# Kernel tuning notes

Hardware: AMD Instinct MI355X
Metric: run time of the kernel (lower is better)

Reference implementation:

```python
import jax, jax.numpy as jnp
import numpy as np

DIST_SCALE = 10000.0   # divisor in kernel()
KERNEL_EPS = 0.0001    # additive epsilon before reciprocal


def setup_inputs() -> dict:
    key = jax.random.key(0)
    k1, k2, k3 = jax.random.split(key, 3)
    batch, keysize, dict_size, categories = 4096, 512, 16384, 128
    x = jax.random.normal(k1, (batch, keysize), dtype=jnp.float32)
    # keras TruncatedNormal(mean=0, stddev=3) approximated by scaled normal
    keys = 3.0 * jax.random.normal(k2, (dict_size, keysize), dtype=jnp.float32)
    V = jax.random.normal(k3, (dict_size, categories), dtype=jnp.float32)
    return {"x": x, "keys": keys, "V": V}


def reference(x, keys, V):
    # sq_distance(keys, x): (dict_size, batch)
    sq = (
        jnp.sum(keys * keys, axis=1, keepdims=True)            # (D, 1)
        - 2.0 * jnp.einsum("dk,bk->db", keys, x)               # (D, B)
        + jnp.sum(x * x, axis=1)[None, :]                      # (1, B)
    )
    kern = 1.0 / (sq / DIST_SCALE + KERNEL_EPS)                # (D, B)
    KV = jnp.einsum("db,dc->bc", kern, V)                      # (B, C)
    # original: diag(1 / (KV @ ones)) @ KV  ==  row-normalize by row sum
    return KV / jnp.sum(KV, axis=1, keepdims=True)
```

## Files before the change

### kernel.cpp

```cpp
#include <hip/hip_runtime.h>

#define BATCH 4096
#define DICT  16384
#define KDIM  512
#define CAT   128
#define ND    16
#define DSLICE (DICT/ND)
#define DCH   64
#define BT    256

typedef __attribute__((ext_vector_type(4))) float          f32x4;
typedef __attribute__((ext_vector_type(8))) short          short8;
typedef __attribute__((ext_vector_type(8))) unsigned short ushort8;

__device__ __forceinline__ unsigned short f2bf(float f) {
  unsigned int u = __float_as_uint(f);
  return (unsigned short)((u + 0x7fffu + ((u >> 16) & 1u)) >> 16);
}

#define AS1 __attribute__((address_space(1)))
#define AS3 __attribute__((address_space(3)))
__device__ __forceinline__ void gl_lds16(const void* g, void* l) {
  __builtin_amdgcn_global_load_lds((AS1 void*)(g), (AS3 void*)(l), 16, 0, 0);
}

template <int N>
__device__ __forceinline__ void waitv() {
  if constexpr (N == 0)      asm volatile("s_waitcnt vmcnt(0)" ::: "memory");
  else if constexpr (N == 5) asm volatile("s_waitcnt vmcnt(5)" ::: "memory");
  else                       asm volatile("s_waitcnt vmcnt(6)" ::: "memory");
  __builtin_amdgcn_sched_barrier(0);
}

#define MFMA16(a, b, c) __builtin_amdgcn_mfma_f32_16x16x32_bf16((a), (b), (c), 0, 0, 0)

__global__ void prep_rows(const float* __restrict__ in,
                          unsigned short* __restrict__ ob,
                          float* __restrict__ sums) {
  const int lane = threadIdx.x & 63, wv = threadIdx.x >> 6;
  const int row = blockIdx.x * 4 + wv;
  const float* rp = in + ((size_t)row << 9);
  float4 a = *(const float4*)(rp + lane * 8);
  float4 b = *(const float4*)(rp + lane * 8 + 4);
  float s = a.x*a.x + a.y*a.y + a.z*a.z + a.w*a.w
          + b.x*b.x + b.y*b.y + b.z*b.z + b.w*b.w;
  ushort8 o;
  o[0]=f2bf(a.x); o[1]=f2bf(a.y); o[2]=f2bf(a.z); o[3]=f2bf(a.w);
  o[4]=f2bf(b.x); o[5]=f2bf(b.y); o[6]=f2bf(b.z); o[7]=f2bf(b.w);
  *(ushort8*)(ob + ((size_t)row << 9) + lane * 8) = o;
  #pragma unroll
  for (int m = 32; m; m >>= 1) s += __shfl_xor(s, m);
  if (lane == 0) sums[row] = s;
}

__global__ void prep_vt(const float* __restrict__ V,
                        unsigned short* __restrict__ Vt) {
  __shared__ float t[64][129];
  const int d0 = blockIdx.x * 64;
  const int tid = threadIdx.x;
  #pragma unroll
  for (int j = 0; j < 32; ++j) {
    int idx = j * 256 + tid;
    t[idx >> 7][idx & 127] = V[((size_t)d0 << 7) + idx];
  }
  __syncthreads();
  #pragma unroll
  for (int j = 0; j < 32; ++j) {
    int idx = j * 256 + tid;
    int cc = idx >> 6, dd = idx & 63;
    Vt[((size_t)cc << 14) + d0 + dd] = f2bf(t[dd][cc]);
  }
}

__global__ __launch_bounds__(512, 2)
void varkeys_fused(const unsigned short* __restrict__ xb,
                   const unsigned short* __restrict__ kb,
                   const unsigned short* __restrict__ vt,
                   const float* __restrict__ sx,
                   const float* __restrict__ sk,
                   float* __restrict__ kvp) {
  __shared__ __attribute__((aligned(16))) char lds[131072];
  char* const VsB = lds + 81920;
  char* const PsB = lds + 98304;

  const int tid  = threadIdx.x;
  const int lane = tid & 63;
  const int wv   = tid >> 6;
  const int c    = lane & 15;
  const int h    = lane >> 4;
  const int sw   = (lane & 7) << 4;
  const int l3   = lane >> 3;

  const int bid    = blockIdx.x;
  const int btile  = bid & 15;
  const int dslice = bid >> 4;
  const int b0     = btile * BT;
  const int dbase  = dslice * DSLICE;

  const float sxv0 = sx[b0 + wv * 32 + c];
  const float sxv1 = sx[b0 + wv * 32 + 16 + c];

  const int rowA  = wv * 8 + l3;
  const int rowB0 = wv * 32 + l3;
  const int ofs   = (((lane & 7) ^ l3) << 4);

  const char* xbB = (const char*)xb;
  const char* kbB = (const char*)kb;
  const char* vtB = (const char*)vt;
  char* const Ps  = PsB + (wv << 12);

  const f32x4 zero = {0.f, 0.f, 0.f, 0.f};
  f32x4 acc[2][8];
  #pragma unroll
  for (int i = 0; i < 2; ++i)
    #pragma unroll
    for (int j = 0; j < 8; ++j) acc[i][j] = zero;

  gl_lds16(kbB + ((size_t)(dbase + rowA) << 10) + ofs, lds + wv * 1024);
  #pragma unroll
  for (int r = 0; r < 4; ++r)
    gl_lds16(xbB + ((size_t)(b0 + rowB0 + r * 8) << 10) + ofs,
             lds + 16384 + (wv * 4 + r) * 1024);

  f32x4 skq[4];

  for (int dc = 0; dc < DSLICE / DCH; ++dc) {
    const int dg = dbase + dc * DCH;

    f32x4 S[4][2];
    #pragma unroll
    for (int i = 0; i < 4; ++i) { S[i][0] = zero; S[i][1] = zero; }

    #pragma unroll
    for (int kk = 0; kk < 8; ++kk) {
      __builtin_amdgcn_s_barrier();
      if (kk == 0) {
        #pragma unroll
        for (int i = 0; i < 4; ++i)
          skq[i] = *(const f32x4*)(sk + dg + i * 16 + h * 4);
      }
      if (!(kk == 7 && dc == (DSLICE / DCH - 1))) {
        const int dg2 = (kk == 7) ? dg + DCH : dg;
        const int kb2 = ((kk + 1) & 7) << 7;
        char* A2 = lds + ((kk + 1) & 1) * 8192;
        char* B2 = lds + 16384 + ((kk + 1) & 1) * 32768;
        gl_lds16(kbB + ((size_t)(dg2 + rowA) << 10) + kb2 + ofs, A2 + wv * 1024);
        #pragma unroll
        for (int r = 0; r < 4; ++r)
          gl_lds16(xbB + ((size_t)(b0 + rowB0 + r * 8) << 10) + kb2 + ofs,
                   B2 + (wv * 4 + r) * 1024);
        if (kk == 3)
          gl_lds16(vtB + ((size_t)(wv * 8 + l3) << 15) + ((size_t)dg << 1) + ofs,
                   VsB + wv * 1024);
        if (kk == 4)
          gl_lds16(vtB + ((size_t)(64 + wv * 8 + l3) << 15) + ((size_t)dg << 1) + ofs,
                   VsB + 8192 + wv * 1024);
      }
      if (kk == 7) { if (dc == DSLICE / DCH - 1) waitv<0>(); else waitv<5>(); }
      else if (kk == 3 || kk == 4) waitv<6>();
      else waitv<5>();
      __builtin_amdgcn_s_barrier();
      __builtin_amdgcn_sched_barrier(0);

      const char* As = lds + (kk & 1) * 8192;
      const char* Bs = lds + 16384 + (kk & 1) * 32768;
      #pragma unroll
      for (int kf = 0; kf < 2; ++kf) {
        const int ko = (kf * 64 + h * 16) ^ sw;
        short8 bf0 = *(const short8*)(Bs + ((wv * 32 + c) << 7) + ko);
        short8 bf1 = *(const short8*)(Bs + ((wv * 32 + 16 + c) << 7) + ko);
        #pragma unroll
        for (int i = 0; i < 4; ++i) {
          short8 af = *(const short8*)(As + ((i * 16 + c) << 7) + ko);
          S[i][0] = MFMA16(af, bf0, S[i][0]);
          S[i][1] = MFMA16(af, bf1, S[i][1]);
        }
      }
    }

    #pragma unroll
    for (int i = 0; i < 4; ++i) {
      const f32x4 skv = skq[i];
      #pragma unroll
      for (int fj = 0; fj < 2; ++fj) {
        const float sxv = fj ? sxv1 : sxv0;
        f32x4 s = S[i][fj];
        float k0 = 10000.f * __builtin_amdgcn_rcpf(skv[0] + sxv - 2.f * s[0] + 1.f);
        float k1 = 10000.f * __builtin_amdgcn_rcpf(skv[1] + sxv - 2.f * s[1] + 1.f);
        float k2 = 10000.f * __builtin_amdgcn_rcpf(skv[2] + sxv - 2.f * s[2] + 1.f);
        float k3 = 10000.f * __builtin_amdgcn_rcpf(skv[3] + sxv - 2.f * s[3] + 1.f);
        unsigned int w0 = (unsigned int)f2bf(k0) | ((unsigned int)f2bf(k1) << 16);
        unsigned int w1 = (unsigned int)f2bf(k2) | ((unsigned int)f2bf(k3) << 16);
        int b = fj * 16 + c;
        char* p = Ps + (b << 7) + ((i * 32 + h * 8) ^ sw);
        ((unsigned int*)p)[0] = w0;
        ((unsigned int*)p)[1] = w1;
      }
    }

    #pragma unroll
    for (int dk = 0; dk < 2; ++dk) {
      const int ko = (dk * 64 + h * 16) ^ sw;
      short8 pa0 = *(const short8*)(Ps + (c << 7) + ko);
      short8 pa1 = *(const short8*)(Ps + ((16 + c) << 7) + ko);
      #pragma unroll
      for (int fc = 0; fc < 8; ++fc) {
        short8 vb = *(const short8*)(VsB + ((fc * 16 + c) << 7) + ko);
        acc[0][fc] = MFMA16(pa0, vb, acc[0][fc]);
        acc[1][fc] = MFMA16(pa1, vb, acc[1][fc]);
      }
    }
  }

  float* op = kvp + (((size_t)dslice * BATCH + b0 + wv * 32) << 7);
  #pragma unroll
  for (int fb = 0; fb < 2; ++fb)
    #pragma unroll
    for (int r = 0; r < 4; ++r) {
      int brow = fb * 16 + h * 4 + r;
      #pragma unroll
      for (int fc = 0; fc < 8; ++fc)
        op[((size_t)brow << 7) + fc * 16 + c] = acc[fb][fc][r];
    }
}

__global__ void reduce_norm(const float* __restrict__ part, float* __restrict__ out) {
  const int lane = threadIdx.x & 63, wv = threadIdx.x >> 6;
  const int b = blockIdx.x * 4 + wv;
  float v0 = 0.f, v1 = 0.f;
  #pragma unroll
  for (int s = 0; s < ND; ++s) {
    const float* p = part + ((((size_t)s << 12) + b) << 7);
    v0 += p[lane]; v1 += p[lane + 64];
  }
  float t = v0 + v1;
  #pragma unroll
  for (int m = 32; m; m >>= 1) t += __shfl_xor(t, m);
  out[((size_t)b << 7) + lane]      = v0 / t;
  out[((size_t)b << 7) + lane + 64] = v1 / t;
}

extern "C" void kernel_launch(void* const* d_in, const int* in_sizes, int n_in,
                              void* d_out, int out_size, void* d_ws, size_t ws_size,
                              hipStream_t stream) {
  (void)in_sizes; (void)n_in; (void)out_size; (void)ws_size;
  const float* x    = (const float*)d_in[0];
  const float* keys = (const float*)d_in[1];
  const float* V    = (const float*)d_in[2];
  float* out = (float*)d_out;
  char* ws = (char*)d_ws;
  unsigned short* xb = (unsigned short*)(ws);
  unsigned short* kb = (unsigned short*)(ws + ((size_t)4 << 20));
  unsigned short* vt = (unsigned short*)(ws + ((size_t)20 << 20));
  float* sx  = (float*)(ws + ((size_t)24 << 20));
  float* sk  = (float*)(ws + ((size_t)24 << 20) + (1 << 16));
  float* kvp = (float*)(ws + ((size_t)25 << 20));

  prep_rows<<<BATCH / 4, 256, 0, stream>>>(x, xb, sx);
  prep_rows<<<DICT / 4, 256, 0, stream>>>(keys, kb, sk);
  prep_vt<<<DICT / 64, 256, 0, stream>>>(V, vt);
  varkeys_fused<<<(BATCH / BT) * ND, 512, 0, stream>>>(xb, kb, vt, sx, sk, kvp);
  reduce_norm<<<BATCH / 4, 256, 0, stream>>>(kvp, out);
}
```

Before: 139.3 us.

## Feed kernel tile straight from registers into second MFMA via permuted V layout

Drops the LDS round trip for the kernel-weight tile P. The S accumulator registers are converted with packed bf16 conversion and used directly as the A operand of the second MFMA. To make the register layout match the reduction index, prep_vt permutes the d ordering of the transposed V. The epilogue also stages accumulators through LDS so the partial-output stores become coalesced 16-byte writes. The cost is an extra barrier and LDS pass at the end, plus reliance on the permutation exactly matching the MFMA fragment layout.

```diff
diff --git a/kernel.cpp b/kernel.cpp
--- a/kernel.cpp
+++ b/kernel.cpp
@@ -12,10 +12,17 @@
 typedef __attribute__((ext_vector_type(4))) float          f32x4;
 typedef __attribute__((ext_vector_type(8))) short          short8;
 typedef __attribute__((ext_vector_type(8))) unsigned short ushort8;
+typedef __attribute__((ext_vector_type(4))) int            intx4;
 
 __device__ __forceinline__ unsigned short f2bf(float f) {
   unsigned int u = __float_as_uint(f);
   return (unsigned short)((u + 0x7fffu + ((u >> 16) & 1u)) >> 16);
+}
+
+__device__ __forceinline__ unsigned int cvtpk_bf16(float lo, float hi) {
+  unsigned int r;
+  asm volatile("v_cvt_pk_bf16_f32 %0, %1, %2" : "=v"(r) : "v"(lo), "v"(hi));
+  return r;
 }
 
 #define AS1 __attribute__((address_space(1)))
@@ -68,7 +75,9 @@
   for (int j = 0; j < 32; ++j) {
     int idx = j * 256 + tid;
     int cc = idx >> 6, dd = idx & 63;
-    Vt[((size_t)cc << 14) + d0 + dd] = f2bf(t[dd][cc]);
+    int p = dd & 31, qq = p >> 3, jj = p & 7;
+    int src = (dd & 32) + 4 * qq + ((jj < 4) ? jj : (12 + jj));
+    Vt[((size_t)cc << 14) + d0 + dd] = f2bf(t[src][cc]);
   }
 }
 
@@ -81,7 +90,6 @@
                    float* __restrict__ kvp) {
   __shared__ __attribute__((aligned(16))) char lds[131072];
   char* const VsB = lds + 81920;
-  char* const PsB = lds + 98304;
 
   const int tid  = threadIdx.x;
   const int lane = tid & 63;
@@ -107,7 +115,6 @@
   const char* xbB = (const char*)xb;
   const char* kbB = (const char*)kb;
   const char* vtB = (const char*)vt;
-  char* const Ps  = PsB + (wv << 12);
 
   const f32x4 zero = {0.f, 0.f, 0.f, 0.f};
   f32x4 acc[2][8];
@@ -179,49 +186,58 @@
     }
 
     #pragma unroll
-    for (int i = 0; i < 4; ++i) {
-      const f32x4 skv = skq[i];
+    for (int dk = 0; dk < 2; ++dk) {
+      short8 pa[2];
       #pragma unroll
       for (int fj = 0; fj < 2; ++fj) {
         const float sxv = fj ? sxv1 : sxv0;
-        f32x4 s = S[i][fj];
-        float k0 = 10000.f * __builtin_amdgcn_rcpf(skv[0] + sxv - 2.f * s[0] + 1.f);
-        float k1 = 10000.f * __builtin_amdgcn_rcpf(skv[1] + sxv - 2.f * s[1] + 1.f);
-        float k2 = 10000.f * __builtin_amdgcn_rcpf(skv[2] + sxv - 2.f * s[2] + 1.f);
-        float k3 = 10000.f * __builtin_amdgcn_rcpf(skv[3] + sxv - 2.f * s[3] + 1.f);
-        unsigned int w0 = (unsigned int)f2bf(k0) | ((unsigned int)f2bf(k1) << 16);
-        unsigned int w1 = (unsigned int)f2bf(k2) | ((unsigned int)f2bf(k3) << 16);
-        int b = fj * 16 + c;
-        char* p = Ps + (b << 7) + ((i * 32 + h * 8) ^ sw);
-        ((unsigned int*)p)[0] = w0;
-        ((unsigned int*)p)[1] = w1;
-      }
-    }
-
-    #pragma unroll
-    for (int dk = 0; dk < 2; ++dk) {
+        const f32x4 sA = S[2 * dk][fj];
+        const f32x4 sB = S[2 * dk + 1][fj];
+        const f32x4 kA = skq[2 * dk];
+        const f32x4 kB = skq[2 * dk + 1];
+        float a0 = 10000.f * __builtin_amdgcn_rcpf(kA[0] + sxv - 2.f * sA[0] + 1.f);
+        float a1 = 10000.f * __builtin_amdgcn_rcpf(kA[1] + sxv - 2.f * sA[1] + 1.f);
+        float a2 = 10000.f * __builtin_amdgcn_rcpf(kA[2] + sxv - 2.f * sA[2] + 1.f);
+        float a3 = 10000.f * __builtin_amdgcn_rcpf(kA[3] + sxv - 2.f * sA[3] + 1.f);
+        float b0f = 10000.f * __builtin_amdgcn_rcpf(kB[0] + sxv - 2.f * sB[0] + 1.f);
+        float b1f = 10000.f * __builtin_amdgcn_rcpf(kB[1] + sxv - 2.f * sB[1] + 1.f);
+        float b2f = 10000.f * __builtin_amdgcn_rcpf(kB[2] + sxv - 2.f * sB[2] + 1.f);
+        float b3f = 10000.f * __builtin_amdgcn_rcpf(kB[3] + sxv - 2.f * sB[3] + 1.f);
+        intx4 fw;
+        fw[0] = (int)cvtpk_bf16(a0, a1);
+        fw[1] = (int)cvtpk_bf16(a2, a3);
+        fw[2] = (int)cvtpk_bf16(b0f, b1f);
+        fw[3] = (int)cvtpk_bf16(b2f, b3f);
+        pa[fj] = *(short8*)&fw;
+      }
       const int ko = (dk * 64 + h * 16) ^ sw;
-      short8 pa0 = *(const short8*)(Ps + (c << 7) + ko);
-      short8 pa1 = *(const short8*)(Ps + ((16 + c) << 7) + ko);
       #pragma unroll
       for (int fc = 0; fc < 8; ++fc) {
         short8 vb = *(const short8*)(VsB + ((fc * 16 + c) << 7) + ko);
-        acc[0][fc] = MFMA16(pa0, vb, acc[0][fc]);
-        acc[1][fc] = MFMA16(pa1, vb, acc[1][fc]);
+        acc[0][fc] = MFMA16(pa[0], vb, acc[0][fc]);
+        acc[1][fc] = MFMA16(pa[1], vb, acc[1][fc]);
       }
     }
   }
 
+  __syncthreads();
+  float* eb = (float*)(lds + (wv << 14));
+  #pragma unroll
+  for (int fb = 0; fb < 2; ++fb)
+    #pragma unroll
+    for (int r = 0; r < 4; ++r) {
+      const int brow = fb * 16 + h * 4 + r;
+      #pragma unroll
+      for (int fc = 0; fc < 8; ++fc)
+        eb[(brow << 7) + fc * 16 + c] = acc[fb][fc][r];
+    }
   float* op = kvp + (((size_t)dslice * BATCH + b0 + wv * 32) << 7);
   #pragma unroll
-  for (int fb = 0; fb < 2; ++fb)
-    #pragma unroll
-    for (int r = 0; r < 4; ++r) {
-      int brow = fb * 16 + h * 4 + r;
-      #pragma unroll
-      for (int fc = 0; fc < 8; ++fc)
-        op[((size_t)brow << 7) + fc * 16 + c] = acc[fb][fc][r];
-    }
+  for (int t = 0; t < 16; ++t) {
+    const int row = t * 2 + (lane >> 5);
+    f32x4 v = *(const f32x4*)(eb + (row << 7) + ((lane & 31) << 2));
+    *(f32x4*)(op + (((size_t)row) << 7) + ((lane & 31) << 2)) = v;
+  }
 }
 
 __global__ void reduce_norm(const float* __restrict__ part, float* __restrict__ out) {
```

Result: faster. 135.1 us (-3.0%).
